# Kernel tuning notes

Measured on AMD Instinct MI355X. Metric: run time of the kernel, lower is better.

## Reference

```python
import jax, jax.numpy as jnp
import numpy as np

B, S, D, H = 2, 2048, 1024, 16
DK = D // H
NEG = -1.0e9


def setup_inputs() -> dict:
    key = jax.random.key(0)
    ks = jax.random.split(key, 11)
    inp = {
        "q": jax.random.normal(ks[0], (B, S, D), jnp.float32),
        "k": jax.random.normal(ks[1], (B, S, D), jnp.float32),
        "v": jax.random.normal(ks[2], (B, S, D), jnp.float32),
        "mask": jnp.tril(jnp.ones((S, S), jnp.int32))[None, None],  # causal [1,1,S,S]
    }
    scale = 0.02
    inp["w_q"] = jax.random.normal(ks[3], (D, D), jnp.float32) * scale
    inp["b_q"] = jnp.zeros((D,), jnp.float32)
    inp["w_k"] = jax.random.normal(ks[4], (D, D), jnp.float32) * scale
    inp["b_k"] = jnp.zeros((D,), jnp.float32)
    inp["w_v"] = jax.random.normal(ks[5], (D, D), jnp.float32) * scale
    inp["b_v"] = jnp.zeros((D,), jnp.float32)
    inp["w_o"] = jax.random.normal(ks[6], (D, D), jnp.float32) * scale
    inp["b_o"] = jnp.zeros((D,), jnp.float32)
    return inp


def reference(q, k, v, mask, w_q, b_q, w_k, b_k, w_v, b_v, w_o, b_o):
    # projections: [B,S,D] -> [B,H,S,DK]
    def proj(x, w, b):
        y = jnp.einsum("bsd,de->bse", x, w) + b
        return y.reshape(B, S, H, DK).transpose(0, 2, 1, 3)

    Q = proj(q, w_q, b_q)
    K = proj(k, w_k, b_k)
    V = proj(v, w_v, b_v)
    # explicit scores matrix, faithful to the original naive attention
    scores = jnp.einsum("bhsd,bhtd->bhst", Q, K) / jnp.sqrt(jnp.float32(DK))
    scores = jnp.where(mask == 0, NEG, scores)
    attn = jax.nn.softmax(scores, axis=-1)  # dropout p=0.0 -> identity
    x = jnp.einsum("bhst,bhtd->bhsd", attn, V)
    x = x.transpose(0, 2, 1, 3).reshape(B, S, D)
    return jnp.einsum("bsd,de->bse", x, w_o) + b_o
```

## Files before the change

kernel.cpp:

```cpp
#include <hip/hip_runtime.h>
#include <hip/hip_bf16.h>

typedef __bf16 bf16;
typedef __bf16 bf16x2 __attribute__((ext_vector_type(2)));
typedef __bf16 bf16x8 __attribute__((ext_vector_type(8)));
typedef float f32x4 __attribute__((ext_vector_type(4)));
typedef float f32x16 __attribute__((ext_vector_type(16)));

#define MFMA16(a, b, c) __builtin_amdgcn_mfma_f32_16x16x32_bf16(a, b, c, 0, 0, 0)
#define MFMA32(a, b, c) __builtin_amdgcn_mfma_f32_32x32x16_bf16(a, b, c, 0, 0, 0)

#define QSCALE 0.18033688f

__device__ __forceinline__ void gld16(const bf16* g, bf16* l) {
  __builtin_amdgcn_global_load_lds(
      (const __attribute__((address_space(1))) void*)g,
      (__attribute__((address_space(3))) void*)l, 16, 0, 0);
}

__global__ __launch_bounds__(256) void prep_k(
    const float* __restrict__ w0, const float* __restrict__ w1,
    const float* __restrict__ w2, const float* __restrict__ w3,
    bf16* __restrict__ dst, const float* __restrict__ q,
    const float* __restrict__ k, const float* __restrict__ v,
    bf16* __restrict__ qb, bf16* __restrict__ kb, bf16* __restrict__ vb) {
  const int t = threadIdx.x;
  if (blockIdx.z >= 4) {
    const int zi = blockIdx.z - 4;
    const float* src = zi == 0 ? q : zi == 1 ? k : v;
    bf16* d = zi == 0 ? qb : zi == 1 ? kb : vb;
    const int fb = blockIdx.y * 16 + blockIdx.x;
#pragma unroll
    for (int j = 0; j < 8; ++j) {
      const size_t i = ((size_t)j * 65536 + fb * 256 + t) * 8;
      float4 a = *(const float4*)(src + i);
      float4 b = *(const float4*)(src + i + 4);
      bf16x8 o;
      o[0] = (bf16)a.x; o[1] = (bf16)a.y; o[2] = (bf16)a.z; o[3] = (bf16)a.w;
      o[4] = (bf16)b.x; o[5] = (bf16)b.y; o[6] = (bf16)b.z; o[7] = (bf16)b.w;
      *(bf16x8*)(d + i) = o;
    }
    return;
  }

  __shared__ bf16 T[64][68];
  const float* W = blockIdx.z == 0 ? w0 : blockIdx.z == 1 ? w1
                   : blockIdx.z == 2 ? w2 : w3;
  bf16* Y = dst + (size_t)blockIdx.z * 1024 * 1024;
  const int r = t >> 2, c4 = t & 3;
  const int k0 = blockIdx.y * 64, n0 = blockIdx.x * 64;

  const float4* src = (const float4*)(W + (size_t)(k0 + r) * 1024 + n0 + c4 * 16);
  float4 f0 = src[0], f1 = src[1], f2 = src[2], f3 = src[3];
  bf16* row = &T[r][c4 * 16];
  row[0] = (bf16)f0.x; row[1] = (bf16)f0.y; row[2] = (bf16)f0.z; row[3] = (bf16)f0.w;
  row[4] = (bf16)f1.x; row[5] = (bf16)f1.y; row[6] = (bf16)f1.z; row[7] = (bf16)f1.w;
  row[8] = (bf16)f2.x; row[9] = (bf16)f2.y; row[10] = (bf16)f2.z; row[11] = (bf16)f2.w;
  row[12] = (bf16)f3.x; row[13] = (bf16)f3.y; row[14] = (bf16)f3.z; row[15] = (bf16)f3.w;
  __syncthreads();

  bf16x8 o0, o1;
#pragma unroll
  for (int j = 0; j < 8; ++j) o0[j] = T[c4 * 16 + j][r];
#pragma unroll
  for (int j = 0; j < 8; ++j) o1[j] = T[c4 * 16 + 8 + j][r];
  bf16* d = Y + (size_t)(n0 + r) * 1024 + k0 + c4 * 16;
  *(bf16x8*)d = o0;
  *(bf16x8*)(d + 8) = o1;
}

template <int QKV, int MT>
__global__ __launch_bounds__(256, 3) void gemm_p(
    const bf16* __restrict__ xq, const bf16* __restrict__ xk,
    const bf16* __restrict__ xv, const bf16* __restrict__ Wt,
    const float* __restrict__ bq, const float* __restrict__ bk,
    const float* __restrict__ bv, bf16* __restrict__ Qp,
    bf16* __restrict__ Kp, bf16* __restrict__ Vtp, float* __restrict__ Yf) {
  constexpr int AROWS = MT * 32;
  __shared__ __align__(16) bf16 SH[AROWS * 64 + 128 * 64];
  bf16* Al = SH;
  bf16* Bl = SH + AROWS * 64;

  const int z = QKV ? blockIdx.z : 0;
  const bf16* X = QKV ? (z == 0 ? xq : z == 1 ? xk : xv) : xq;
  const bf16* Bt = Wt + (size_t)z * 1048576;
  const float* bias = QKV ? (z == 0 ? bq : z == 1 ? bk : bv) : bq;
  const float escale = (QKV && z == 0) ? QSCALE : 1.0f;

  const int t = threadIdx.x;
  const int wave = t >> 6, lane = t & 63, quad = lane >> 4, l16 = lane & 15;
  const int wm = (wave >> 1) * (MT * 16), wn = (wave & 1) * 64;
  const int bm = blockIdx.y * AROWS, bn = blockIdx.x * 128;

  const int lr = (lane >> 3) & 7, lc = lane & 7;
  constexpr int NAC = AROWS / 32;
  const bf16* gA[NAC];
  bf16* lA[NAC];
#pragma unroll
  for (int i = 0; i < NAC; ++i) {
    const int q = wave * NAC + i;
    gA[i] = X + (size_t)(bm + 8 * q + lr) * 1024 + 8 * (lc ^ lr);
    lA[i] = Al + q * 512;
  }
  const bf16* gB[4];
  bf16* lB[4];
#pragma unroll
  for (int i = 0; i < 4; ++i) {
    const int q = wave * 4 + i;
    gB[i] = Bt + (size_t)(bn + 8 * q + lr) * 1024 + 8 * (lc ^ lr);
    lB[i] = Bl + q * 512;
  }

  f32x4 acc[MT][4] = {};
  const int fswz = (l16 & 7) << 4;

  for (int kb = 0; kb < 1024; kb += 64) {
    __syncthreads();
#pragma unroll
    for (int i = 0; i < NAC; ++i) gld16(gA[i] + kb, lA[i]);
#pragma unroll
    for (int i = 0; i < 4; ++i) gld16(gB[i] + kb, lB[i]);
    __syncthreads();

#pragma unroll
    for (int kk = 0; kk < 2; ++kk) {
      const int cb = (kk * 64 + quad * 16) ^ fswz;
      bf16x8 af[MT], bfr[4];
#pragma unroll
      for (int mt = 0; mt < MT; ++mt)
        af[mt] = *(const bf16x8*)((const char*)Al +
                                  (wm + mt * 16 + l16) * 128 + cb);
#pragma unroll
      for (int nt = 0; nt < 4; ++nt)
        bfr[nt] = *(const bf16x8*)((const char*)Bl +
                                   (wn + nt * 16 + l16) * 128 + cb);
#pragma unroll
      for (int mt = 0; mt < MT; ++mt)
#pragma unroll
        for (int nt = 0; nt < 4; ++nt)
          acc[mt][nt] = MFMA16(af[mt], bfr[nt], acc[mt][nt]);
    }
  }

  if (QKV && z == 2) {
    bf16* Tt = SH;
    const int b = bm >> 11;
    __syncthreads();
#pragma unroll
    for (int half = 0; half < 2; ++half) {
      if ((wave & 1) == half) {
#pragma unroll
        for (int nt = 0; nt < 4; ++nt) {
          const int ln = nt * 16 + l16;
          const float bia = bias[bn + half * 64 + ln];
#pragma unroll
          for (int mt = 0; mt < 4; ++mt)
#pragma unroll
            for (int r = 0; r < 4; ++r) {
              const int m = wm + mt * 16 + quad * 4 + r;
              Tt[ln * 136 + m] = (bf16)(acc[mt][nt][r] + bia);
            }
        }
      }
      __syncthreads();
      {
        const int ln = t >> 2, seg = (t & 3) * 32;
        const int gn = bn + half * 64 + ln;
        const int h = gn >> 6, dk = gn & 63;
        const int s0 = (bm & 2047) + seg;
        bf16* dstp = Vtp + ((size_t)(b * 16 + h) * 64 + dk) * 2048 + s0;
        const bf16* srcp = Tt + ln * 136 + seg;
#pragma unroll
        for (int j = 0; j < 4; ++j)
          *(bf16x8*)(dstp + j * 8) = *(const bf16x8*)(srcp + j * 8);
      }
      __syncthreads();
    }
  } else {
#pragma unroll
    for (int mt = 0; mt < MT; ++mt)
#pragma unroll
      for (int nt = 0; nt < 4; ++nt) {
        const int gn = bn + wn + nt * 16 + l16;
        const float bia = bias[gn];
#pragma unroll
        for (int r = 0; r < 4; ++r) {
          const int gm = bm + wm + mt * 16 + quad * 4 + r;
          const float val = (acc[mt][nt][r] + bia) * escale;
          if (!QKV) {
            Yf[(size_t)gm * 1024 + gn] = val;
          } else {
            const int b = gm >> 11, s = gm & 2047;
            const int h = gn >> 6, dk = gn & 63;
            bf16* Y = (z == 0) ? Qp : Kp;
            Y[((size_t)(b * 16 + h) * 2048 + s) * 64 + dk] = (bf16)val;
          }
        }
      }
  }
}

__global__ __launch_bounds__(512, 4) void attn_k(const bf16* __restrict__ Q,
                                                 const bf16* __restrict__ K,
                                                 const bf16* __restrict__ Vt,
                                                 bf16* __restrict__ X) {
  __shared__ float Ex[3][2][1024];
  __shared__ float ExR[3][2][64];
  __shared__ float rsL[2][32];

  const int t = threadIdx.x;
  const int wave = t >> 6, lane = t & 63;
  const int cl = lane & 31, h = lane >> 5;
  const int qsub = wave & 1, kp = wave >> 1;

  const int n = blockIdx.x;
  const int xcd = n & 7, mm = n >> 3;
  const int bh = xcd + 8 * (mm & 3);
  const int pairx = mm >> 2;
  const int b = bh >> 4, hh = bh & 15;

  const bf16* Qb = Q + (size_t)bh * 2048 * 64;
  const bf16* Kb = K + (size_t)bh * 2048 * 64;
  const bf16* Vb = Vt + (size_t)bh * 64 * 2048;

  for (int ph = 0; ph < 2; ++ph) {
    const int qt = ph ? 31 - pairx : pairx;
    const int ntiles = qt + 1;
    const int q0 = qt * 64 + qsub * 32;

    bf16x8 qf[4];
#pragma unroll
    for (int ks = 0; ks < 4; ++ks)
      qf[ks] = *(const bf16x8*)(Qb + (size_t)(q0 + cl) * 64 + ks * 16 + h * 8);

    f32x16 o0 = {}, o1 = {};
    float rs = 0.f;

    for (int kt = kp; kt < ntiles; kt += 4) {
      const int k0 = kt * 64;
      const bool interior = (k0 + 63) <= q0;

      const bf16* Kt0 = Kb + (size_t)(k0 + cl) * 64 + h * 8;
      const bf16* Kt1 = Kb + (size_t)(k0 + cl + 32) * 64 + h * 8;
      bf16x8 kf0[4], kf1[4];
#pragma unroll
      for (int ks = 0; ks < 4; ++ks) {
        kf0[ks] = *(const bf16x8*)(Kt0 + ks * 16);
        kf1[ks] = *(const bf16x8*)(Kt1 + ks * 16);
      }
      f32x16 s0v = {}, s1v = {};
#pragma unroll
      for (int ks = 0; ks < 4; ++ks) {
        s0v = MFMA32(kf0[ks], qf[ks], s0v);
        s1v = MFMA32(kf1[ks], qf[ks], s1v);
      }

      const bf16* Vr0 = Vb + (size_t)cl * 2048 + k0 + h * 8;
      const bf16* Vr1 = Vb + (size_t)(cl + 32) * 2048 + k0 + h * 8;
      bf16x8 vf0[4], vf1[4];
#pragma unroll
      for (int ks = 0; ks < 4; ++ks) {
        vf0[ks] = *(const bf16x8*)(Vr0 + ks * 16);
        vf1[ks] = *(const bf16x8*)(Vr1 + ks * 16);
      }

      unsigned pk[8][2];
      float ts = 0.f;
      auto smax = [&](const f32x16& sv, int mk) {
#pragma unroll
        for (int sl = 0; sl < 4; ++sl)
#pragma unroll
          for (int p = 0; p < 2; ++p) {
            float e0 = exp2f(sv[sl * 4 + 2 * p]);
            float e1 = exp2f(sv[sl * 4 + 2 * p + 1]);
            if (!interior) {
              const int ky = k0 + mk * 32 + 8 * sl + 4 * h + 2 * p;
              const int qg = q0 + cl;
              if (ky > qg) e0 = 0.f;
              if (ky + 1 > qg) e1 = 0.f;
            }
            ts += e0 + e1;
            union { bf16x2 v; unsigned u; } cv;
            cv.v[0] = (bf16)e0;
            cv.v[1] = (bf16)e1;
            pk[mk * 4 + sl][p] = cv.u;
          }
      };
      smax(s0v, 0);
      smax(s1v, 1);
      rs += ts;

      bf16x8 pf[4];
#pragma unroll
      for (int ks = 0; ks < 4; ++ks) {
        const unsigned oe0 = pk[2 * ks][0], oe1 = pk[2 * ks][1];
        const unsigned oo0 = pk[2 * ks + 1][0], oo1 = pk[2 * ks + 1][1];
        const unsigned pe0 = (unsigned)__shfl_xor((int)oe0, 32, 64);
        const unsigned pe1 = (unsigned)__shfl_xor((int)oe1, 32, 64);
        const unsigned po0 = (unsigned)__shfl_xor((int)oo0, 32, 64);
        const unsigned po1 = (unsigned)__shfl_xor((int)oo1, 32, 64);
        union { unsigned u[4]; bf16x8 v; } fu;
        fu.u[0] = h ? po0 : oe0;
        fu.u[1] = h ? po1 : oe1;
        fu.u[2] = h ? oo0 : pe0;
        fu.u[3] = h ? oo1 : pe1;
        pf[ks] = fu.v;
      }

#pragma unroll
      for (int ks = 0; ks < 4; ++ks) {
        o0 = MFMA32(pf[ks], vf0[ks], o0);
        o1 = MFMA32(pf[ks], vf1[ks], o1);
      }
    }

    if (kp > 0) {
      float* e = &Ex[kp - 1][qsub][0];
#pragma unroll
      for (int i = 0; i < 16; ++i) e[i * 64 + lane] = o0[i];
      ExR[kp - 1][qsub][lane] = rs;
    }
    __syncthreads();
    if (kp == 0) {
#pragma unroll
      for (int w = 0; w < 3; ++w) {
        const float* e = &Ex[w][qsub][0];
#pragma unroll
        for (int i = 0; i < 16; ++i) o0[i] += e[i * 64 + lane];
        rs += ExR[w][qsub][lane];
      }
    }
    __syncthreads();
    if (kp > 0) {
      float* e = &Ex[kp - 1][qsub][0];
#pragma unroll
      for (int i = 0; i < 16; ++i) e[i * 64 + lane] = o1[i];
    }
    __syncthreads();
    if (kp == 0) {
#pragma unroll
      for (int w = 0; w < 3; ++w) {
        const float* e = &Ex[w][qsub][0];
#pragma unroll
        for (int i = 0; i < 16; ++i) o1[i] += e[i * 64 + lane];
      }

      const float rtot = rs + __shfl_xor(rs, 32, 64);
      rsL[qsub][cl] = 1.0f / rtot;
      __builtin_amdgcn_s_waitcnt(0xC07F);
      bf16* Xb = X + (size_t)b * 2048 * 1024 + hh * 64;
#pragma unroll
      for (int g = 0; g < 16; ++g) {
        const int qr = (g & 3) + 8 * (g >> 2) + 4 * h;
        const float ri = rsL[qsub][qr];
        const int qg = q0 + qr;
        Xb[(size_t)qg * 1024 + cl] = (bf16)(o0[g] * ri);
        Xb[(size_t)qg * 1024 + 32 + cl] = (bf16)(o1[g] * ri);
      }
    }
    __syncthreads();
  }
}

extern "C" void kernel_launch(void* const* d_in, const int* in_sizes, int n_in,
                              void* d_out, int out_size, void* d_ws,
                              size_t ws_size, hipStream_t stream) {
  const float* q = (const float*)d_in[0];
  const float* k = (const float*)d_in[1];
  const float* v = (const float*)d_in[2];
  const float* w_q = (const float*)d_in[4];
  const float* b_q = (const float*)d_in[5];
  const float* w_k = (const float*)d_in[6];
  const float* b_k = (const float*)d_in[7];
  const float* w_v = (const float*)d_in[8];
  const float* b_v = (const float*)d_in[9];
  const float* w_o = (const float*)d_in[10];
  const float* b_o = (const float*)d_in[11];

  bf16* ws = (bf16*)d_ws;
  const size_t NELEM = (size_t)4096 * 1024;
  bf16* Qp = ws;
  bf16* Kp = ws + NELEM;
  bf16* Vtp = ws + 2 * NELEM;
  bf16* Xp = ws + 3 * NELEM;
  bf16* Wt = ws + 4 * NELEM;
  bf16* Wto = Wt + 3145728;
  bf16* qb = Xp;
  bf16* kb = (bf16*)d_out;
  bf16* vb = kb + NELEM;

  prep_k<<<dim3(16, 16, 7), 256, 0, stream>>>(w_q, w_k, w_v, w_o, Wt, q, k, v,
                                              qb, kb, vb);

  gemm_p<1, 4><<<dim3(8, 32, 3), 256, 0, stream>>>(
      qb, kb, vb, Wt, b_q, b_k, b_v, Qp, Kp, Vtp, nullptr);
  attn_k<<<dim3(512), 512, 0, stream>>>(Qp, Kp, Vtp, Xp);
  gemm_p<0, 2><<<dim3(8, 64), 256, 0, stream>>>(
      Xp, nullptr, nullptr, Wto, b_o, nullptr, nullptr, nullptr, nullptr,
      nullptr, (float*)d_out);
}
```

Before: 265.1 us.

## Stage K/V tiles in swizzled LDS via async global-to-LDS loads in attention

```diff
diff --git a/kernel.cpp b/kernel.cpp
--- a/kernel.cpp
+++ b/kernel.cpp
@@ -204,9 +204,13 @@
                                                  const bf16* __restrict__ K,
                                                  const bf16* __restrict__ Vt,
                                                  bf16* __restrict__ X) {
-  __shared__ float Ex[3][2][1024];
+  __shared__ __align__(16) char LB[65536];
+  __shared__ float Ex[3][2][512];
   __shared__ float ExR[3][2][64];
   __shared__ float rsL[2][32];
+
+  bf16* KB = (bf16*)LB;
+  bf16* VB = (bf16*)(LB + 32768);
 
   const int t = threadIdx.x;
   const int wave = t >> 6, lane = t & 63;
@@ -223,9 +227,21 @@
   const bf16* Kb = K + (size_t)bh * 2048 * 64;
   const bf16* Vb = Vt + (size_t)bh * 64 * 2048;
 
+  const int lr = (lane >> 3) & 7, lc = lane & 7;
+  const int st = wave & 3;
+  const bool isV = wave >= 4;
+  const bf16* gsb = isV ? (Vb + (size_t)lr * 2048 + 8 * (lc ^ lr))
+                        : (Kb + (size_t)lr * 64 + 8 * (lc ^ lr));
+  const size_t cqStep = isV ? 16384 : 512;
+  const size_t ktStep = isV ? 64 : 4096;
+  bf16* lbs = (isV ? VB : KB) + st * 4096;
+
+  const int fswz = (cl & 7) << 4;
+
   for (int ph = 0; ph < 2; ++ph) {
     const int qt = ph ? 31 - pairx : pairx;
     const int ntiles = qt + 1;
+    const int S = (ntiles + 3) >> 2;
     const int q0 = qt * 64 + qsub * 32;
 
     bf16x8 qf[4];
@@ -236,88 +252,92 @@
     f32x16 o0 = {}, o1 = {};
     float rs = 0.f;
 
-    for (int kt = kp; kt < ntiles; kt += 4) {
-      const int k0 = kt * 64;
-      const bool interior = (k0 + 63) <= q0;
-
-      const bf16* Kt0 = Kb + (size_t)(k0 + cl) * 64 + h * 8;
-      const bf16* Kt1 = Kb + (size_t)(k0 + cl + 32) * 64 + h * 8;
-      bf16x8 kf0[4], kf1[4];
-#pragma unroll
-      for (int ks = 0; ks < 4; ++ks) {
-        kf0[ks] = *(const bf16x8*)(Kt0 + ks * 16);
-        kf1[ks] = *(const bf16x8*)(Kt1 + ks * 16);
-      }
-      f32x16 s0v = {}, s1v = {};
-#pragma unroll
-      for (int ks = 0; ks < 4; ++ks) {
-        s0v = MFMA32(kf0[ks], qf[ks], s0v);
-        s1v = MFMA32(kf1[ks], qf[ks], s1v);
-      }
-
-      const bf16* Vr0 = Vb + (size_t)cl * 2048 + k0 + h * 8;
-      const bf16* Vr1 = Vb + (size_t)(cl + 32) * 2048 + k0 + h * 8;
-      bf16x8 vf0[4], vf1[4];
-#pragma unroll
-      for (int ks = 0; ks < 4; ++ks) {
-        vf0[ks] = *(const bf16x8*)(Vr0 + ks * 16);
-        vf1[ks] = *(const bf16x8*)(Vr1 + ks * 16);
-      }
-
-      unsigned pk[8][2];
-      float ts = 0.f;
-      auto smax = [&](const f32x16& sv, int mk) {
-#pragma unroll
-        for (int sl = 0; sl < 4; ++sl)
-#pragma unroll
-          for (int p = 0; p < 2; ++p) {
-            float e0 = exp2f(sv[sl * 4 + 2 * p]);
-            float e1 = exp2f(sv[sl * 4 + 2 * p + 1]);
-            if (!interior) {
-              const int ky = k0 + mk * 32 + 8 * sl + 4 * h + 2 * p;
-              const int qg = q0 + cl;
-              if (ky > qg) e0 = 0.f;
-              if (ky + 1 > qg) e1 = 0.f;
+    for (int ss = 0; ss < S; ++ss) {
+      const int stt = 4 * ss + st;
+      if (stt < ntiles) {
+#pragma unroll
+        for (int cq = 0; cq < 8; ++cq)
+          gld16(gsb + (size_t)stt * ktStep + cq * cqStep, lbs + cq * 512);
+      }
+      __syncthreads();
+
+      const int kt = 4 * ss + kp;
+      if (kt < ntiles) {
+        const int k0 = kt * 64;
+        const char* Kc = (const char*)(KB + kp * 4096);
+        const char* Vc = (const char*)(VB + kp * 4096);
+        const bool interior = (k0 + 63) <= q0;
+
+        f32x16 s0v = {}, s1v = {};
+#pragma unroll
+        for (int ks = 0; ks < 4; ++ks) {
+          const int cb = ks * 32 + h * 16;
+          bf16x8 f0 = *(const bf16x8*)(Kc + cl * 128 + (cb ^ fswz));
+          bf16x8 f1 = *(const bf16x8*)(Kc + (cl + 32) * 128 + (cb ^ fswz));
+          s0v = MFMA32(f0, qf[ks], s0v);
+          s1v = MFMA32(f1, qf[ks], s1v);
+        }
+
+        unsigned pk[8][2];
+        float ts = 0.f;
+        auto smax = [&](const f32x16& sv, int mk) {
+#pragma unroll
+          for (int sl = 0; sl < 4; ++sl)
+#pragma unroll
+            for (int p = 0; p < 2; ++p) {
+              float e0 = exp2f(sv[sl * 4 + 2 * p]);
+              float e1 = exp2f(sv[sl * 4 + 2 * p + 1]);
+              if (!interior) {
+                const int ky = k0 + mk * 32 + 8 * sl + 4 * h + 2 * p;
+                const int qg = q0 + cl;
+                if (ky > qg) e0 = 0.f;
+                if (ky + 1 > qg) e1 = 0.f;
+              }
+              ts += e0 + e1;
+              union { bf16x2 v; unsigned u; } cv;
+              cv.v[0] = (bf16)e0;
+              cv.v[1] = (bf16)e1;
+              pk[mk * 4 + sl][p] = cv.u;
             }
-            ts += e0 + e1;
-            union { bf16x2 v; unsigned u; } cv;
-            cv.v[0] = (bf16)e0;
-            cv.v[1] = (bf16)e1;
-            pk[mk * 4 + sl][p] = cv.u;
-          }
-      };
-      smax(s0v, 0);
-      smax(s1v, 1);
-      rs += ts;
-
-      bf16x8 pf[4];
-#pragma unroll
-      for (int ks = 0; ks < 4; ++ks) {
-        const unsigned oe0 = pk[2 * ks][0], oe1 = pk[2 * ks][1];
-        const unsigned oo0 = pk[2 * ks + 1][0], oo1 = pk[2 * ks + 1][1];
-        const unsigned pe0 = (unsigned)__shfl_xor((int)oe0, 32, 64);
-        const unsigned pe1 = (unsigned)__shfl_xor((int)oe1, 32, 64);
-        const unsigned po0 = (unsigned)__shfl_xor((int)oo0, 32, 64);
-        const unsigned po1 = (unsigned)__shfl_xor((int)oo1, 32, 64);
-        union { unsigned u[4]; bf16x8 v; } fu;
-        fu.u[0] = h ? po0 : oe0;
-        fu.u[1] = h ? po1 : oe1;
-        fu.u[2] = h ? oo0 : pe0;
-        fu.u[3] = h ? oo1 : pe1;
-        pf[ks] = fu.v;
-      }
-
-#pragma unroll
-      for (int ks = 0; ks < 4; ++ks) {
-        o0 = MFMA32(pf[ks], vf0[ks], o0);
-        o1 = MFMA32(pf[ks], vf1[ks], o1);
-      }
+        };
+        smax(s0v, 0);
+        smax(s1v, 1);
+        rs += ts;
+
+        bf16x8 pf[4];
+#pragma unroll
+        for (int ks = 0; ks < 4; ++ks) {
+          const unsigned oe0 = pk[2 * ks][0], oe1 = pk[2 * ks][1];
+          const unsigned oo0 = pk[2 * ks + 1][0], oo1 = pk[2 * ks + 1][1];
+          const unsigned pe0 = (unsigned)__shfl_xor((int)oe0, 32, 64);
+          const unsigned pe1 = (unsigned)__shfl_xor((int)oe1, 32, 64);
+          const unsigned po0 = (unsigned)__shfl_xor((int)oo0, 32, 64);
+          const unsigned po1 = (unsigned)__shfl_xor((int)oo1, 32, 64);
+          union { unsigned u[4]; bf16x8 v; } fu;
+          fu.u[0] = h ? po0 : oe0;
+          fu.u[1] = h ? po1 : oe1;
+          fu.u[2] = h ? oo0 : pe0;
+          fu.u[3] = h ? oo1 : pe1;
+          pf[ks] = fu.v;
+        }
+
+#pragma unroll
+        for (int ks = 0; ks < 4; ++ks) {
+          const int cb = ks * 32 + h * 16;
+          bf16x8 v0f = *(const bf16x8*)(Vc + cl * 128 + (cb ^ fswz));
+          bf16x8 v1f = *(const bf16x8*)(Vc + (cl + 32) * 128 + (cb ^ fswz));
+          o0 = MFMA32(pf[ks], v0f, o0);
+          o1 = MFMA32(pf[ks], v1f, o1);
+        }
+      }
+
+      __syncthreads();
     }
 
     if (kp > 0) {
       float* e = &Ex[kp - 1][qsub][0];
 #pragma unroll
-      for (int i = 0; i < 16; ++i) e[i * 64 + lane] = o0[i];
+      for (int i = 0; i < 8; ++i) e[i * 64 + lane] = o0[i];
       ExR[kp - 1][qsub][lane] = rs;
     }
     __syncthreads();
@@ -326,7 +346,7 @@
       for (int w = 0; w < 3; ++w) {
         const float* e = &Ex[w][qsub][0];
 #pragma unroll
-        for (int i = 0; i < 16; ++i) o0[i] += e[i * 64 + lane];
+        for (int i = 0; i < 8; ++i) o0[i] += e[i * 64 + lane];
         rs += ExR[w][qsub][lane];
       }
     }
@@ -334,7 +354,7 @@
     if (kp > 0) {
       float* e = &Ex[kp - 1][qsub][0];
 #pragma unroll
-      for (int i = 0; i < 16; ++i) e[i * 64 + lane] = o1[i];
+      for (int i = 0; i < 8; ++i) e[i * 64 + lane] = o0[8 + i];
     }
     __syncthreads();
     if (kp == 0) {
@@ -342,7 +362,37 @@
       for (int w = 0; w < 3; ++w) {
         const float* e = &Ex[w][qsub][0];
 #pragma unroll
-        for (int i = 0; i < 16; ++i) o1[i] += e[i * 64 + lane];
+        for (int i = 0; i < 8; ++i) o0[8 + i] += e[i * 64 + lane];
+      }
+    }
+    __syncthreads();
+    if (kp > 0) {
+      float* e = &Ex[kp - 1][qsub][0];
+#pragma unroll
+      for (int i = 0; i < 8; ++i) e[i * 64 + lane] = o1[i];
+    }
+    __syncthreads();
+    if (kp == 0) {
+#pragma unroll
+      for (int w = 0; w < 3; ++w) {
+        const float* e = &Ex[w][qsub][0];
+#pragma unroll
+        for (int i = 0; i < 8; ++i) o1[i] += e[i * 64 + lane];
+      }
+    }
+    __syncthreads();
+    if (kp > 0) {
+      float* e = &Ex[kp - 1][qsub][0];
+#pragma unroll
+      for (int i = 0; i < 8; ++i) e[i * 64 + lane] = o1[8 + i];
+    }
+    __syncthreads();
+    if (kp == 0) {
+#pragma unroll
+      for (int w = 0; w < 3; ++w) {
+        const float* e = &Ex[w][qsub][0];
+#pragma unroll
+        for (int i = 0; i < 8; ++i) o1[8 + i] += e[i * 64 + lane];
       }
 
       const float rtot = rs + __shfl_xor(rs, 32, 64);
```

Result: faster. 245.9 us (-7.2%).
